# Kernel tuning notes

Hardware: AMD Instinct MI355X
Metric: run time of the kernel (lower is better)

The kernel has to match this reference:

```python
import jax, jax.numpy as jnp
import numpy as np

B, D, T = 16, 64, 3000
N_CB, K = 8, 1024


def setup_inputs() -> dict:
    key = jax.random.key(0)
    k1, k2 = jax.random.split(key)
    x = jax.random.normal(k1, (B, D, T), dtype=jnp.float32)
    embeds = jax.random.normal(k2, (N_CB, K, D), dtype=jnp.float32) * 0.02
    return {"x": x, "embeds": embeds}


def _vq_stage(r_flat, embed):
    """One VectorQuantize layer on flattened [N, D] input (eval mode).

    Returns (quantized_st [N,D], indices [N], commit+codebook loss, utilization).
    """
    # squared Euclidean distances [N, K]; argmin is identical to cdist argmin
    d2 = (jnp.sum(r_flat * r_flat, axis=-1, keepdims=True)
          - 2.0 * (r_flat @ embed.T)
          + jnp.sum(embed * embed, axis=-1))
    idx = jnp.argmin(d2, axis=-1)                      # [N]
    q = embed[idx]                                     # [N, D] gather
    sg = jax.lax.stop_gradient
    commit = jnp.mean((r_flat - sg(q)) ** 2)
    codebook = jnp.mean((q - sg(r_flat)) ** 2)
    q_st = r_flat + sg(q - r_flat)                     # straight-through
    used = jnp.zeros((K,), dtype=jnp.float32).at[idx].set(1.0)
    util = jnp.sum(used) / K                           # == len(unique)/K
    return q_st, idx, commit + codebook, util


def reference(x, embeds):
    """ResidualVQ forward (eval mode): x [B, D, T], embeds [n_cb, K, D]."""
    sg = jax.lax.stop_gradient
    residual = x
    quantized_total = jnp.zeros_like(x)
    all_indices = []
    total_commit = jnp.float32(0.0)
    total_util = jnp.float32(0.0)
    for i in range(N_CB):
        r_flat = residual.transpose(0, 2, 1).reshape(-1, D)  # [B*T, D]
        q_st_flat, idx, commit, util = _vq_stage(r_flat, embeds[i])
        q_st = q_st_flat.reshape(x.shape[0], x.shape[2], D).transpose(0, 2, 1)
        residual = residual - sg(q_st)
        quantized_total = quantized_total + q_st
        all_indices.append(idx)
        total_commit = total_commit + commit
        total_util = total_util + util
    indices = jnp.stack(all_indices, axis=0)           # [n_cb, B*T]
    return quantized_total, indices, total_commit / N_CB, total_util / N_CB
```

## Files before the change

### kernel.cpp

```cpp
#include <hip/hip_runtime.h>
#include <hip/hip_bf16.h>
#include <math.h>

#define Bn   16
#define Dn   64
#define Tn   3000
#define Nn   (Bn*Tn)
#define NCB  8
#define Kn   1024
#define KTB  64
#define NCHK (Kn/KTB)
#define NTB  64
#define NBLK (Nn/NTB)
#define QMAX 512

#define SM_RH   0
#define SM_RL   8192
#define SM_EH   16384
#define SM_RF   24576
#define SM_SE   40960
#define SM_SR   41216
#define SM_BEST 41472
#define SM_QCNT 41984
#define SM_QUE  42000
#define SM_BK   44048
#define SM_TOT  44304

#define WS_EHI   12288000
#define WS_SE    13336576
#define WS_USED  13369344
#define WS_LOSS  13402112
#define WS_SEMAX 13402128

#define OUT_QT_OFF  0
#define OUT_IDX_OFF 3072000
#define OUT_SC_OFF  3456000

typedef __attribute__((ext_vector_type(4))) float f32x4;
typedef __attribute__((ext_vector_type(8))) short s16x8;

__device__ __forceinline__ unsigned short f2bf(float x) {
    unsigned int u = __float_as_uint(x);
    unsigned int r = (u + 0x7FFFu + ((u >> 16) & 1u)) >> 16;
    return (unsigned short)r;
}
__device__ __forceinline__ float bf2f(unsigned short h) {
    return __uint_as_float(((unsigned int)h) << 16);
}

__global__ void vq_se(const float* __restrict__ emb, float* __restrict__ se,
                      float* __restrict__ semax)
{
    int r = blockIdx.x * 256 + threadIdx.x;
    if (r < NCB*Kn) {
        const float* p = emb + r*Dn;
        float a0=0.f, a1=0.f, a2=0.f, a3=0.f;
        #pragma unroll
        for (int d = 0; d < Dn; d += 4) {
            a0 = fmaf(p[d+0], p[d+0], a0);
            a1 = fmaf(p[d+1], p[d+1], a1);
            a2 = fmaf(p[d+2], p[d+2], a2);
            a3 = fmaf(p[d+3], p[d+3], a3);
        }
        float v = (a0+a1)+(a2+a3);
        se[r] = v;
        atomicMax((int*)&semax[r >> 10], __float_as_int(v));
    }
}

__global__ void vq_ebf(const float* __restrict__ emb, char* __restrict__ ehi)
{
    int idx = blockIdx.x * 256 + threadIdx.x;
    int r = idx >> 3;
    int s = idx & 7;
    const float* p = emb + (size_t)r*Dn + s*8;
    s16x8 hh;
    #pragma unroll
    for (int j = 0; j < 8; ++j) hh[j] = (short)f2bf(p[j]);
    int cb = r >> 10, kk = r & 1023, c = kk >> 6, kl = kk & 63;
    size_t off = (size_t)cb*131072 + (size_t)c*8192 + (size_t)kl*128 + ((s ^ (kl & 7)) << 4);
    *(s16x8*)(ehi + off) = hh;
}

__device__ __forceinline__
float vq_rescore(const float* rf, float sr, float sek,
                 const float* __restrict__ emb_cb, int n, int kg)
{
    const float4* ep = (const float4*)(emb_cb + (size_t)kg*Dn);
    float q0=0.f,q1=0.f,q2=0.f,q3=0.f;
    #pragma unroll 4
    for (int m = 0; m < 16; ++m) {
        float4 e4 = ep[m];
        q0 = fmaf(rf[(4*m+0)*64 + n], e4.x, q0);
        q1 = fmaf(rf[(4*m+1)*64 + n], e4.y, q1);
        q2 = fmaf(rf[(4*m+2)*64 + n], e4.z, q2);
        q3 = fmaf(rf[(4*m+3)*64 + n], e4.w, q3);
    }
    float dot = (q0+q1)+(q2+q3);
    return (sr - 2.0f*dot) + sek;
}

__global__ __launch_bounds__(256, 3)
void vq_mega(const float* __restrict__ x, const float* __restrict__ emb,
             const char* __restrict__ ehib, const float* __restrict__ se_g,
             const float* __restrict__ semax_g,
             float* __restrict__ out_qt, float* __restrict__ out_idx,
             float* __restrict__ used_g, float* __restrict__ loss_acc)
{
    __shared__ __align__(16) char smem[SM_TOT];
    float*  rf     = (float*)(smem + SM_RF);
    float*  selds  = (float*)(smem + SM_SE);
    float*  lds_sr = (float*)(smem + SM_SR);
    unsigned long long* best64 = (unsigned long long*)(smem + SM_BEST);
    int*    qcnt   = (int*)(smem + SM_QCNT);
    unsigned int* que = (unsigned int*)(smem + SM_QUE);
    float*  srpart = (float*)(smem + SM_QUE);
    int*    bkL    = (int*)(smem + SM_BK);

    const int tid = threadIdx.x;
    const int n0 = blockIdx.x * NTB;
    const int lane = tid & 63, w = tid >> 6;
    const int lrow = lane & 15, lhi = lane >> 4;
    const int nl = tid & 63;
    const int dg = tid >> 6;
    const float4* hsrc = (const float4*)ehib;

    {
        const int n = n0 + nl;
        const int b = n / Tn, t = n % Tn;
        const float* gp = x + b*(Dn*Tn) + t;
        float v[16];
        #pragma unroll
        for (int j = 0; j < 16; ++j) v[j] = gp[(dg*16 + j)*Tn];
        float a0=0.f,a1=0.f,a2=0.f,a3=0.f;
        #pragma unroll
        for (int j = 0; j < 16; j += 4) {
            a0 = fmaf(v[j+0], v[j+0], a0);
            a1 = fmaf(v[j+1], v[j+1], a1);
            a2 = fmaf(v[j+2], v[j+2], a2);
            a3 = fmaf(v[j+3], v[j+3], a3);
        }
        srpart[dg*64 + nl] = (a0+a1)+(a2+a3);
        unsigned short hi[16], lo[16];
        #pragma unroll
        for (int j = 0; j < 16; ++j) {
            rf[(dg*16 + j)*64 + nl] = v[j];
            hi[j] = f2bf(v[j]);
            lo[j] = f2bf(v[j] - bf2f(hi[j]));
        }
        s16x8 ph0, ph1, pl0, pl1;
        #pragma unroll
        for (int j = 0; j < 8; ++j) {
            ph0[j] = (short)hi[j];   ph1[j] = (short)hi[j+8];
            pl0[j] = (short)lo[j];   pl1[j] = (short)lo[j+8];
        }
        const int s0 = dg*2, s1 = dg*2 + 1, nx = nl & 7;
        *(s16x8*)(smem + SM_RH + nl*128 + ((s0 ^ nx) << 4)) = ph0;
        *(s16x8*)(smem + SM_RH + nl*128 + ((s1 ^ nx) << 4)) = ph1;
        *(s16x8*)(smem + SM_RL + nl*128 + ((s0 ^ nx) << 4)) = pl0;
        *(s16x8*)(smem + SM_RL + nl*128 + ((s1 ^ nx) << 4)) = pl1;
    }
    if (tid < 64) best64[tid] = ~0ULL;
    if (tid == 0) qcnt[0] = 0;
    __syncthreads();
    if (tid < 64)
        lds_sr[tid] = (srpart[tid] + srpart[64+tid]) + (srpart[128+tid] + srpart[192+tid]);
    ((float4*)(smem + SM_EH))[tid]       = hsrc[tid];
    ((float4*)(smem + SM_EH))[tid+256]   = hsrc[tid+256];
    if (tid < KTB) selds[tid] = se_g[tid];

    float lsum = 0.f;
    const int nlocal = w*16 + lrow;

    for (int s = 0; s < NCB; ++s) {
        const float* emb_s = emb + (size_t)s*(Kn*Dn);
        const float semx = semax_g[s];
        float m_run = INFINITY;
        float band = 0.f;

        for (int c = 0; c < NCHK; ++c) {
            __syncthreads();
            if (c == 0)
                band = 0.0095f * sqrtf(semx * lds_sr[nlocal]) + 2e-4f;

            const bool pre = (c < NCHK-1) || (s < NCB-1);
            float4 h0, h1; float sepre = 0.f;
            if (pre) {
                size_t nb = (c < NCHK-1) ? ((size_t)s*8192 + (size_t)(c+1)*512)
                                         : ((size_t)(s+1)*8192);
                h0 = hsrc[nb + tid]; h1 = hsrc[nb + 256 + tid];
                if (tid < KTB)
                    sepre = se_g[(c < NCHK-1) ? (s*Kn + (c+1)*KTB + tid)
                                              : ((s+1)*Kn + tid)];
            }

            f32x4 acc[4];
            #pragma unroll
            for (int i = 0; i < 4; ++i) acc[i] = (f32x4){0.f,0.f,0.f,0.f};
            #pragma unroll
            for (int ks = 0; ks < 2; ++ks) {
                const int sdim = ks*4 + lhi;
                const int swz = ((sdim ^ (lrow & 7)) << 4);
                const size_t roff = (size_t)(w*16 + lrow)*128 + swz;
                const size_t eoff = (size_t)lrow*128 + swz;
                s16x8 bh = *(const s16x8*)(smem + SM_RH + roff);
                s16x8 bl = *(const s16x8*)(smem + SM_RL + roff);
                #pragma unroll
                for (int i = 0; i < 4; ++i) {
                    s16x8 ah = *(const s16x8*)(smem + SM_EH + eoff + i*2048);
                    acc[i] = __builtin_amdgcn_mfma_f32_16x16x32_bf16(ah, bh, acc[i], 0, 0, 0);
                    acc[i] = __builtin_amdgcn_mfma_f32_16x16x32_bf16(ah, bl, acc[i], 0, 0, 0);
                }
            }

            float mi[4];
            float m = INFINITY;
            #pragma unroll
            for (int i = 0; i < 4; ++i) {
                #pragma unroll
                for (int rg = 0; rg < 4; ++rg)
                    acc[i][rg] = selds[i*16 + lhi*4 + rg] - 2.0f*acc[i][rg];
                float a = fminf(fminf(acc[i][0], acc[i][1]), fminf(acc[i][2], acc[i][3]));
                mi[i] = a;
                m = fminf(m, a);
            }
            m = fminf(m, __shfl_xor(m, 16, 64));
            m = fminf(m, __shfl_xor(m, 32, 64));
            const float thr = fminf(m_run, m) + band;
            m_run = fminf(m_run, m);

            #pragma unroll
            for (int i = 0; i < 4; ++i) {
                if (__any(mi[i] <= thr)) {
                    #pragma unroll
                    for (int rg = 0; rg < 4; ++rg) {
                        if (acc[i][rg] <= thr) {
                            int kl = i*16 + lhi*4 + rg;
                            int kg = c*KTB + kl;
                            int slot = atomicAdd(qcnt, 1);
                            if (slot < QMAX) {
                                que[slot] = ((unsigned)nlocal << 10) | (unsigned)kg;
                            } else {
                                float d2e = vq_rescore(rf, lds_sr[nlocal], selds[kl],
                                                       emb_s, nlocal, kg);
                                unsigned long long pk =
                                    ((unsigned long long)__float_as_uint(d2e) << 32) | (unsigned)kg;
                                atomicMin(&best64[nlocal], pk);
                            }
                        }
                    }
                }
            }
            __syncthreads();
            if (pre) {
                ((float4*)(smem + SM_EH))[tid]     = h0;
                ((float4*)(smem + SM_EH))[tid+256] = h1;
                if (tid < KTB) selds[tid] = sepre;
            }
        }

        const int cnt = min(qcnt[0], QMAX);
        for (int e = tid; e < cnt; e += 256) {
            unsigned ent = que[e];
            int nn = (int)(ent >> 10);
            int kg = (int)(ent & 1023);
            float sek = se_g[s*Kn + kg];
            float d2e = vq_rescore(rf, lds_sr[nn], sek, emb_s, nn, kg);
            unsigned long long pk =
                ((unsigned long long)__float_as_uint(d2e) << 32) | (unsigned)kg;
            atomicMin(&best64[nn], pk);
        }
        __syncthreads();

        if (tid < 64) {
            int bk = (int)(best64[tid] & 0xFFFFFFFFull) & (Kn - 1);
            bkL[tid] = bk;
            out_idx[s*Nn + n0 + tid] = (float)bk;
            used_g[s*Kn + bk] = 1.0f;
            best64[tid] = ~0ULL;
        }
        if (tid == 0) qcnt[0] = 0;
        __syncthreads();

        const float* ep = emb_s + (size_t)bkL[nl]*Dn;
        if (s < NCB-1) {
            float nv[16];
            #pragma unroll
            for (int j = 0; j < 16; ++j) {
                int d = dg*16 + j;
                float rv = rf[d*64 + nl];
                float q  = ep[d];
                float diff = rv - q;
                lsum = fmaf(diff, diff, lsum);
                float qst = rv + (q - rv);
                nv[j] = rv - qst;
                rf[d*64 + nl] = nv[j];
            }
            float a0=0.f,a1=0.f,a2=0.f,a3=0.f;
            #pragma unroll
            for (int j = 0; j < 16; j += 4) {
                a0 = fmaf(nv[j+0], nv[j+0], a0);
                a1 = fmaf(nv[j+1], nv[j+1], a1);
                a2 = fmaf(nv[j+2], nv[j+2], a2);
                a3 = fmaf(nv[j+3], nv[j+3], a3);
            }
            srpart[dg*64 + nl] = (a0+a1)+(a2+a3);
            unsigned short hi[16], lo[16];
            #pragma unroll
            for (int j = 0; j < 16; ++j) {
                hi[j] = f2bf(nv[j]);
                lo[j] = f2bf(nv[j] - bf2f(hi[j]));
            }
            s16x8 ph0, ph1, pl0, pl1;
            #pragma unroll
            for (int j = 0; j < 8; ++j) {
                ph0[j] = (short)hi[j];   ph1[j] = (short)hi[j+8];
                pl0[j] = (short)lo[j];   pl1[j] = (short)lo[j+8];
            }
            const int s0 = dg*2, s1 = dg*2 + 1, nx = nl & 7;
            *(s16x8*)(smem + SM_RH + nl*128 + ((s0 ^ nx) << 4)) = ph0;
            *(s16x8*)(smem + SM_RH + nl*128 + ((s1 ^ nx) << 4)) = ph1;
            *(s16x8*)(smem + SM_RL + nl*128 + ((s0 ^ nx) << 4)) = pl0;
            *(s16x8*)(smem + SM_RL + nl*128 + ((s1 ^ nx) << 4)) = pl1;
            __syncthreads();
            if (tid < 64)
                lds_sr[tid] = (srpart[tid] + srpart[64+tid])
                            + (srpart[128+tid] + srpart[192+tid]);
        } else {
            const int n = n0 + nl;
            const int b = n / Tn, t = n % Tn;
            const float* xp = x + b*(Dn*Tn) + t;
            float* qp = out_qt + b*(Dn*Tn) + t;
            #pragma unroll
            for (int j = 0; j < 16; ++j) {
                int d = dg*16 + j;
                float rv = rf[d*64 + nl];
                float q  = ep[d];
                float diff = rv - q;
                lsum = fmaf(diff, diff, lsum);
                float qst = rv + (q - rv);
                float rn = rv - qst;
                qp[d*Tn] = xp[d*Tn] - rn;
            }
        }
    }

    float* red = (float*)(smem + SM_QUE);
    red[tid] = lsum;
    __syncthreads();
    for (int s2 = 128; s2 > 0; s2 >>= 1) {
        if (tid < s2) red[tid] += red[tid + s2];
        __syncthreads();
    }
    if (tid == 0) atomicAdd(loss_acc, red[0]);
}

__global__ void vq_scalars(const float* __restrict__ used, const float* __restrict__ loss_acc,
                           float* __restrict__ out)
{
    __shared__ float red[256];
    float s = 0.f;
    for (int j = threadIdx.x; j < NCB*Kn; j += 256) s += used[j];
    red[threadIdx.x] = s;
    __syncthreads();
    for (int st = 128; st > 0; st >>= 1) {
        if (threadIdx.x < st) red[threadIdx.x] += red[threadIdx.x + st];
        __syncthreads();
    }
    if (threadIdx.x == 0) {
        float sumsq = loss_acc[0];
        float total_loss = 2.0f * sumsq / (float)(Nn*Dn);
        out[OUT_SC_OFF + 0] = total_loss / (float)NCB;
        out[OUT_SC_OFF + 1] = red[0] / (float)(NCB*Kn);
    }
}

extern "C" void kernel_launch(void* const* d_in, const int* in_sizes, int n_in,
                              void* d_out, int out_size, void* d_ws, size_t ws_size,
                              hipStream_t stream)
{
    const float* x      = (const float*)d_in[0];
    const float* embeds = (const float*)d_in[1];
    float* out = (float*)d_out;
    char* ws = (char*)d_ws;

    char*  ehi   = ws + WS_EHI;
    float* se    = (float*)(ws + WS_SE);
    float* used  = (float*)(ws + WS_USED);
    float* loss  = (float*)(ws + WS_LOSS);
    float* semax = (float*)(ws + WS_SEMAX);

    hipMemsetAsync(used, 0, (size_t)NCB*Kn*sizeof(float) + 48, stream);

    vq_se<<<(NCB*Kn + 255)/256, 256, 0, stream>>>(embeds, se, semax);
    vq_ebf<<<256, 256, 0, stream>>>(embeds, ehi);

    vq_mega<<<NBLK, 256, 0, stream>>>(x, embeds, ehi, se, semax,
                                      out + OUT_QT_OFF, out + OUT_IDX_OFF,
                                      used, loss);

    vq_scalars<<<1, 256, 0, stream>>>(used, loss, out);
}
```

Baseline: 402.9 us.

## Load codebook MFMA fragments directly from global, drop LDS staging and per-chunk barriers

Re-lays out the bf16 codebook in global memory so each lane can load its MFMA A-fragments directly into registers, and removes the LDS double-buffer of codebook chunks along with the two __syncthreads per chunk. The per-stage squared norms of all 1024 codes are staged once into LDS, which replaces per-chunk se loads and the global se read in rescoring. This aims to cut barrier and LDS traffic in the hot chunk loop, at the cost of exposing global/L2 load latency per chunk without explicit prefetch.

```diff
diff --git a/kernel.cpp b/kernel.cpp
--- a/kernel.cpp
+++ b/kernel.cpp
@@ -14,17 +14,16 @@
 #define NBLK (Nn/NTB)
 #define QMAX 512
 
-#define SM_RH   0
-#define SM_RL   8192
-#define SM_EH   16384
-#define SM_RF   24576
-#define SM_SE   40960
-#define SM_SR   41216
-#define SM_BEST 41472
-#define SM_QCNT 41984
-#define SM_QUE  42000
-#define SM_BK   44048
-#define SM_TOT  44304
+#define SM_RH    0
+#define SM_RL    8192
+#define SM_RF    16384
+#define SM_SESTG 32768
+#define SM_SR    36864
+#define SM_BEST  37120
+#define SM_QCNT  37632
+#define SM_QUE   37648
+#define SM_BK    39696
+#define SM_TOT   39952
 
 #define WS_EHI   12288000
 #define WS_SE    13336576
@@ -72,13 +71,15 @@
 {
     int idx = blockIdx.x * 256 + threadIdx.x;
     int r = idx >> 3;
-    int s = idx & 7;
-    const float* p = emb + (size_t)r*Dn + s*8;
+    int sdim = idx & 7;
+    const float* p = emb + (size_t)r*Dn + sdim*8;
     s16x8 hh;
     #pragma unroll
     for (int j = 0; j < 8; ++j) hh[j] = (short)f2bf(p[j]);
     int cb = r >> 10, kk = r & 1023, c = kk >> 6, kl = kk & 63;
-    size_t off = (size_t)cb*131072 + (size_t)c*8192 + (size_t)kl*128 + ((s ^ (kl & 7)) << 4);
+    int i = kl >> 4, lrow = kl & 15, ks = sdim >> 2, lhi = sdim & 3;
+    size_t off = (size_t)cb*131072 + (size_t)c*8192
+               + (size_t)((i*2 + ks)*16 + lrow)*64 + lhi*16;
     *(s16x8*)(ehi + off) = hh;
 }
 
@@ -109,7 +110,7 @@
 {
     __shared__ __align__(16) char smem[SM_TOT];
     float*  rf     = (float*)(smem + SM_RF);
-    float*  selds  = (float*)(smem + SM_SE);
+    float*  sestg  = (float*)(smem + SM_SESTG);
     float*  lds_sr = (float*)(smem + SM_SR);
     unsigned long long* best64 = (unsigned long long*)(smem + SM_BEST);
     int*    qcnt   = (int*)(smem + SM_QCNT);
@@ -123,7 +124,7 @@
     const int lrow = lane & 15, lhi = lane >> 4;
     const int nl = tid & 63;
     const int dg = tid >> 6;
-    const float4* hsrc = (const float4*)ehib;
+    const int laneoff = lrow*64 + lhi*16;
 
     {
         const int n = n0 + nl;
@@ -165,34 +166,27 @@
     __syncthreads();
     if (tid < 64)
         lds_sr[tid] = (srpart[tid] + srpart[64+tid]) + (srpart[128+tid] + srpart[192+tid]);
-    ((float4*)(smem + SM_EH))[tid]       = hsrc[tid];
-    ((float4*)(smem + SM_EH))[tid+256]   = hsrc[tid+256];
-    if (tid < KTB) selds[tid] = se_g[tid];
+    *(float4*)&sestg[tid*4] = *(const float4*)&se_g[tid*4];
+    __syncthreads();
 
     float lsum = 0.f;
     const int nlocal = w*16 + lrow;
 
     for (int s = 0; s < NCB; ++s) {
         const float* emb_s = emb + (size_t)s*(Kn*Dn);
+        const char*  eh_s  = ehib + (size_t)s*131072;
         const float semx = semax_g[s];
+        const float band = 0.0095f * sqrtf(semx * lds_sr[nlocal]) + 2e-4f;
         float m_run = INFINITY;
-        float band = 0.f;
 
         for (int c = 0; c < NCHK; ++c) {
-            __syncthreads();
-            if (c == 0)
-                band = 0.0095f * sqrtf(semx * lds_sr[nlocal]) + 2e-4f;
-
-            const bool pre = (c < NCHK-1) || (s < NCB-1);
-            float4 h0, h1; float sepre = 0.f;
-            if (pre) {
-                size_t nb = (c < NCHK-1) ? ((size_t)s*8192 + (size_t)(c+1)*512)
-                                         : ((size_t)(s+1)*8192);
-                h0 = hsrc[nb + tid]; h1 = hsrc[nb + 256 + tid];
-                if (tid < KTB)
-                    sepre = se_g[(c < NCHK-1) ? (s*Kn + (c+1)*KTB + tid)
-                                              : ((s+1)*Kn + tid)];
-            }
+            const char* ec = eh_s + ((size_t)c << 13);
+            s16x8 ahf[2][4];
+            #pragma unroll
+            for (int ks = 0; ks < 2; ++ks)
+                #pragma unroll
+                for (int i = 0; i < 4; ++i)
+                    ahf[ks][i] = *(const s16x8*)(ec + (((i<<1) + ks) << 10) + laneoff);
 
             f32x4 acc[4];
             #pragma unroll
@@ -202,14 +196,12 @@
                 const int sdim = ks*4 + lhi;
                 const int swz = ((sdim ^ (lrow & 7)) << 4);
                 const size_t roff = (size_t)(w*16 + lrow)*128 + swz;
-                const size_t eoff = (size_t)lrow*128 + swz;
                 s16x8 bh = *(const s16x8*)(smem + SM_RH + roff);
                 s16x8 bl = *(const s16x8*)(smem + SM_RL + roff);
                 #pragma unroll
                 for (int i = 0; i < 4; ++i) {
-                    s16x8 ah = *(const s16x8*)(smem + SM_EH + eoff + i*2048);
-                    acc[i] = __builtin_amdgcn_mfma_f32_16x16x32_bf16(ah, bh, acc[i], 0, 0, 0);
-                    acc[i] = __builtin_amdgcn_mfma_f32_16x16x32_bf16(ah, bl, acc[i], 0, 0, 0);
+                    acc[i] = __builtin_amdgcn_mfma_f32_16x16x32_bf16(ahf[ks][i], bh, acc[i], 0, 0, 0);
+                    acc[i] = __builtin_amdgcn_mfma_f32_16x16x32_bf16(ahf[ks][i], bl, acc[i], 0, 0, 0);
                 }
             }
 
@@ -217,9 +209,10 @@
             float m = INFINITY;
             #pragma unroll
             for (int i = 0; i < 4; ++i) {
+                f32x4 se4 = *(const f32x4*)&sestg[c*64 + i*16 + lhi*4];
                 #pragma unroll
                 for (int rg = 0; rg < 4; ++rg)
-                    acc[i][rg] = selds[i*16 + lhi*4 + rg] - 2.0f*acc[i][rg];
+                    acc[i][rg] = se4[rg] - 2.0f*acc[i][rg];
                 float a = fminf(fminf(acc[i][0], acc[i][1]), fminf(acc[i][2], acc[i][3]));
                 mi[i] = a;
                 m = fminf(m, a);
@@ -241,7 +234,7 @@
                             if (slot < QMAX) {
                                 que[slot] = ((unsigned)nlocal << 10) | (unsigned)kg;
                             } else {
-                                float d2e = vq_rescore(rf, lds_sr[nlocal], selds[kl],
+                                float d2e = vq_rescore(rf, lds_sr[nlocal], sestg[kg],
                                                        emb_s, nlocal, kg);
                                 unsigned long long pk =
                                     ((unsigned long long)__float_as_uint(d2e) << 32) | (unsigned)kg;
@@ -251,21 +244,15 @@
                     }
                 }
             }
-            __syncthreads();
-            if (pre) {
-                ((float4*)(smem + SM_EH))[tid]     = h0;
-                ((float4*)(smem + SM_EH))[tid+256] = h1;
-                if (tid < KTB) selds[tid] = sepre;
-            }
-        }
+        }
+        __syncthreads();
 
         const int cnt = min(qcnt[0], QMAX);
         for (int e = tid; e < cnt; e += 256) {
             unsigned ent = que[e];
             int nn = (int)(ent >> 10);
             int kg = (int)(ent & 1023);
-            float sek = se_g[s*Kn + kg];
-            float d2e = vq_rescore(rf, lds_sr[nn], sek, emb_s, nn, kg);
+            float d2e = vq_rescore(rf, lds_sr[nn], sestg[kg], emb_s, nn, kg);
             unsigned long long pk =
                 ((unsigned long long)__float_as_uint(d2e) << 32) | (unsigned)kg;
             atomicMin(&best64[nn], pk);
@@ -326,6 +313,8 @@
             if (tid < 64)
                 lds_sr[tid] = (srpart[tid] + srpart[64+tid])
                             + (srpart[128+tid] + srpart[192+tid]);
+            *(float4*)&sestg[tid*4] = *(const float4*)&se_g[(s+1)*Kn + tid*4];
+            __syncthreads();
         } else {
             const int n = n0 + nl;
             const int b = n / Tn, t = n % Tn;
```

Result: faster. 385.8 us (-4.2%).
